# Performance work log

Hardware: AMD Instinct MI355X
Metric: run time of the kernel (lower is better)

## Reference

```python
import jax, jax.numpy as jnp
import numpy as np

QMIN_A, QMAX_A = -128, 127  # int8 activation range
GROUPSIZE = 32


def per_token_quant_dequant(x):
    """Dynamic per-token asymmetric int8 fake-quant (torchao per_token_dynamic_quant)."""
    min_val = jnp.minimum(jnp.min(x, axis=-1, keepdims=True), 0.0)
    max_val = jnp.maximum(jnp.max(x, axis=-1, keepdims=True), 0.0)
    scale = (max_val - min_val) / float(QMAX_A - QMIN_A)
    scale = jnp.maximum(scale, jnp.finfo(x.dtype).eps)
    zp = jnp.clip(QMIN_A - jnp.round(min_val / scale), QMIN_A, QMAX_A)
    q = jnp.clip(jnp.round(x / scale) + zp, QMIN_A, QMAX_A)
    return (q - zp) * scale


def dequant_int4_grouped(w_int, w_scales, w_zeros):
    """w_int: [O, I] int4 values in [-8, 7]; scales/zeros: [O, I//GROUPSIZE]."""
    O, I = w_int.shape
    G = I // GROUPSIZE
    wg = w_int.reshape(O, G, GROUPSIZE).astype(w_scales.dtype)
    w_dq = (wg - w_zeros[:, :, None]) * w_scales[:, :, None]
    return w_dq.reshape(O, I)


def setup_inputs() -> dict:
    key = jax.random.key(0)
    k1, k2, k3 = jax.random.split(key, 3)
    B, S, D_IN, D_OUT = 4, 2048, 2048, 2048
    G = D_IN // GROUPSIZE
    x = jax.random.normal(k1, (B, S, D_IN), dtype=jnp.float32)
    w_int = jax.random.randint(k2, (D_OUT, D_IN), -8, 8, dtype=jnp.int32)
    w_scales = jax.random.uniform(k3, (D_OUT, G), dtype=jnp.float32) * 0.01 + 1e-3
    w_zeros = jnp.zeros((D_OUT, G), dtype=jnp.float32)
    return {"x": x, "w_int": w_int, "w_scales": w_scales, "w_zeros": w_zeros}


def reference(x, w_int, w_scales, w_zeros):
    x_dq = per_token_quant_dequant(x)                  # [B, S, I]
    w_dq = dequant_int4_grouped(w_int, w_scales, w_zeros)  # [O, I]
    return jnp.einsum("bsi,oi->bso", x_dq, w_dq)       # [B, S, O]
```

## Files before the change

### kernel.cpp

```cpp
#include <hip/hip_runtime.h>

#define M_DIM 8192
#define N_DIM 2048
#define K_DIM 2048

#define BM 256
#define BN 128
#define BK 64

#define AS1 __attribute__((address_space(1)))
#define AS3 __attribute__((address_space(3)))

typedef float f32x4 __attribute__((ext_vector_type(4)));
typedef short s16x8 __attribute__((ext_vector_type(8)));

__device__ __forceinline__ unsigned short f2bf(float f) {
  unsigned int u = __float_as_uint(f);
  u += 0x7FFFu + ((u >> 16) & 1u);
  return (unsigned short)(u >> 16);
}

__global__ __launch_bounds__(256) void quant_x_kernel(
    const float* __restrict__ x, unsigned short* __restrict__ A) {
  const int t   = blockIdx.x;
  const int tid = threadIdx.x;
  const float4* r4 = (const float4*)(x + (size_t)t * K_DIM);
  float4 v0 = r4[tid];
  float4 v1 = r4[tid + 256];

  float mn = fminf(fminf(fminf(v0.x, v0.y), fminf(v0.z, v0.w)),
                   fminf(fminf(v1.x, v1.y), fminf(v1.z, v1.w)));
  float mx = fmaxf(fmaxf(fmaxf(v0.x, v0.y), fmaxf(v0.z, v0.w)),
                   fmaxf(fmaxf(v1.x, v1.y), fmaxf(v1.z, v1.w)));
#pragma unroll
  for (int off = 32; off > 0; off >>= 1) {
    mn = fminf(mn, __shfl_xor(mn, off));
    mx = fmaxf(mx, __shfl_xor(mx, off));
  }
  __shared__ float smn[4], smx[4];
  if ((tid & 63) == 0) { smn[tid >> 6] = mn; smx[tid >> 6] = mx; }
  __syncthreads();
  mn = fminf(fminf(smn[0], smn[1]), fminf(smn[2], smn[3]));
  mx = fmaxf(fmaxf(smx[0], smx[1]), fmaxf(smx[2], smx[3]));
  mn = fminf(mn, 0.0f);
  mx = fmaxf(mx, 0.0f);

  float scale = (mx - mn) / 255.0f;
  scale = fmaxf(scale, 1.1920928955078125e-07f);
  const float inv = 1.0f / scale;
  float zp = -128.0f - rintf(mn * inv);
  zp = fminf(fmaxf(zp, -128.0f), 127.0f);

  ushort4* Ao = (ushort4*)(A + (size_t)t * K_DIM);
  {
    float q; ushort4 r;
    q = rintf(v0.x * inv) + zp; q = fminf(fmaxf(q, -128.f), 127.f); r.x = f2bf((q - zp) * scale);
    q = rintf(v0.y * inv) + zp; q = fminf(fmaxf(q, -128.f), 127.f); r.y = f2bf((q - zp) * scale);
    q = rintf(v0.z * inv) + zp; q = fminf(fmaxf(q, -128.f), 127.f); r.z = f2bf((q - zp) * scale);
    q = rintf(v0.w * inv) + zp; q = fminf(fmaxf(q, -128.f), 127.f); r.w = f2bf((q - zp) * scale);
    Ao[tid] = r;
  }
  {
    float q; ushort4 r;
    q = rintf(v1.x * inv) + zp; q = fminf(fmaxf(q, -128.f), 127.f); r.x = f2bf((q - zp) * scale);
    q = rintf(v1.y * inv) + zp; q = fminf(fmaxf(q, -128.f), 127.f); r.y = f2bf((q - zp) * scale);
    q = rintf(v1.z * inv) + zp; q = fminf(fmaxf(q, -128.f), 127.f); r.z = f2bf((q - zp) * scale);
    q = rintf(v1.w * inv) + zp; q = fminf(fmaxf(q, -128.f), 127.f); r.w = f2bf((q - zp) * scale);
    Ao[tid + 256] = r;
  }
}

__global__ __launch_bounds__(256) void prep_w_kernel(
    const int* __restrict__ w, const float* __restrict__ ws,
    const float* __restrict__ wz, unsigned short* __restrict__ W) {
  const int idx = blockIdx.x * 256 + threadIdx.x;
  const int o  = idx >> 8;
  const int ii = (idx & 255) * 8;
  const int g  = ii >> 5;
  const float s = ws[o * 64 + g];
  const float z = wz[o * 64 + g];
  const int4* wp = (const int4*)(w + (size_t)o * K_DIM + ii);
  int4 a = wp[0], b = wp[1];
  ushort4 r0, r1;
  r0.x = f2bf(((float)a.x - z) * s);
  r0.y = f2bf(((float)a.y - z) * s);
  r0.z = f2bf(((float)a.z - z) * s);
  r0.w = f2bf(((float)a.w - z) * s);
  r1.x = f2bf(((float)b.x - z) * s);
  r1.y = f2bf(((float)b.y - z) * s);
  r1.z = f2bf(((float)b.z - z) * s);
  r1.w = f2bf(((float)b.w - z) * s);
  ushort4* Wo = (ushort4*)(W + (size_t)o * K_DIM + ii);
  Wo[0] = r0;
  Wo[1] = r1;
}

__global__ __launch_bounds__(256, 2) void gemm_kernel(
    const unsigned short* __restrict__ A,
    const unsigned short* __restrict__ B,
    float* __restrict__ C) {
  __shared__ unsigned short As[BM * BK];
  __shared__ unsigned short Bs[BN * BK];

  const int tid  = threadIdx.x;
  const int bm   = blockIdx.y * BM;
  const int bn   = blockIdx.x * BN;
  const int lane = tid & 63;
  const int wv   = tid >> 6;
  const int waveM = (wv >> 1) * 128;
  const int waveN = (wv & 1) * 64;
  const int quad = lane >> 4;
  const int l16  = lane & 15;

  const int trow = tid >> 3;
  const int phys = (tid & 7) ^ (trow & 7);
  const unsigned short* ag = A + (size_t)(bm + trow) * K_DIM + phys * 8;
  const unsigned short* bg = B + (size_t)(bn + trow) * K_DIM + phys * 8;
  unsigned short* al = &As[tid * 8];
  unsigned short* bl = &Bs[tid * 8];

  int aoff[8], boff[4];
#pragma unroll
  for (int mi = 0; mi < 8; ++mi)
    aoff[mi] = (waveM + mi * 16 + l16) * BK + ((quad ^ (l16 & 7)) * 8);
#pragma unroll
  for (int ni = 0; ni < 4; ++ni)
    boff[ni] = (waveN + ni * 16 + l16) * BK + ((quad ^ (l16 & 7)) * 8);

  f32x4 acc[8][4] = {};

  for (int k0 = 0; k0 < K_DIM; k0 += BK) {
#pragma unroll
    for (int j = 0; j < 8; ++j)
      __builtin_amdgcn_global_load_lds((const AS1 void*)(ag + (size_t)j * 32 * K_DIM + k0),
                                       (AS3 void*)(al + j * 2048), 16, 0, 0);
#pragma unroll
    for (int j = 0; j < 4; ++j)
      __builtin_amdgcn_global_load_lds((const AS1 void*)(bg + (size_t)j * 32 * K_DIM + k0),
                                       (AS3 void*)(bl + j * 2048), 16, 0, 0);
    __syncthreads();

#pragma unroll
    for (int kk = 0; kk < 2; ++kk) {
      s16x8 af[8], bf[4];
#pragma unroll
      for (int mi = 0; mi < 8; ++mi)
        af[mi] = *(const s16x8*)&As[aoff[mi] ^ (kk * 32)];
#pragma unroll
      for (int ni = 0; ni < 4; ++ni)
        bf[ni] = *(const s16x8*)&Bs[boff[ni] ^ (kk * 32)];
#pragma unroll
      for (int mi = 0; mi < 8; ++mi)
#pragma unroll
        for (int ni = 0; ni < 4; ++ni)
          acc[mi][ni] = __builtin_amdgcn_mfma_f32_16x16x32_bf16(
              af[mi], bf[ni], acc[mi][ni], 0, 0, 0);
    }
    __syncthreads();
  }

#pragma unroll
  for (int mi = 0; mi < 8; ++mi) {
#pragma unroll
    for (int ni = 0; ni < 4; ++ni) {
      const int o = bn + waveN + ni * 16 + l16;
#pragma unroll
      for (int r = 0; r < 4; ++r) {
        const int t = bm + waveM + mi * 16 + quad * 4 + r;
        C[(size_t)t * N_DIM + o] = acc[mi][ni][r];
      }
    }
  }
}

extern "C" void kernel_launch(void* const* d_in, const int* in_sizes, int n_in,
                              void* d_out, int out_size, void* d_ws, size_t ws_size,
                              hipStream_t stream) {
  const float* x        = (const float*)d_in[0];
  const int*   w_int    = (const int*)d_in[1];
  const float* w_scales = (const float*)d_in[2];
  const float* w_zeros  = (const float*)d_in[3];
  float* out = (float*)d_out;

  unsigned short* Aq = (unsigned short*)d_ws;
  unsigned short* Wq = Aq + (size_t)M_DIM * K_DIM;

  quant_x_kernel<<<M_DIM, 256, 0, stream>>>(x, Aq);
  prep_w_kernel<<<(N_DIM * (K_DIM / 8)) / 256, 256, 0, stream>>>(w_int, w_scales, w_zeros, Wq);
  dim3 grid(N_DIM / BN, M_DIM / BM);
  gemm_kernel<<<grid, 256, 0, stream>>>(Aq, Wq, out);
}
```

Measured before the change: 195.1 us.

## Double-buffer A tile, register-stage B tile, and swizzle block order

The GEMM main loop now prefetches the next K-slice while computing the current one. A is double-buffered in LDS via direct global-to-LDS loads, and B is loaded into registers and written to LDS after compute behind an extra barrier. Block indices are remapped so neighbouring workgroups share A/B tiles in cache. LDS use grows to about 80KB and register pressure rises, which may hurt the 2-blocks-per-CU occupancy target.

```diff
diff --git a/kernel.cpp b/kernel.cpp
--- a/kernel.cpp
+++ b/kernel.cpp
@@ -99,12 +99,15 @@
     const unsigned short* __restrict__ A,
     const unsigned short* __restrict__ B,
     float* __restrict__ C) {
-  __shared__ unsigned short As[BM * BK];
+  __shared__ unsigned short As[2 * BM * BK];
   __shared__ unsigned short Bs[BN * BK];
 
   const int tid  = threadIdx.x;
-  const int bm   = blockIdx.y * BM;
-  const int bn   = blockIdx.x * BN;
+  const int id  = blockIdx.y * 16 + blockIdx.x;
+  const int nid = (id & 7) * 64 + (id >> 3);
+  const int bm  = (nid >> 4) * BM;
+  const int bn  = (nid & 15) * BN;
+
   const int lane = tid & 63;
   const int wv   = tid >> 6;
   const int waveM = (wv >> 1) * 128;
@@ -115,9 +118,14 @@
   const int trow = tid >> 3;
   const int phys = (tid & 7) ^ (trow & 7);
   const unsigned short* ag = A + (size_t)(bm + trow) * K_DIM + phys * 8;
-  const unsigned short* bg = B + (size_t)(bn + trow) * K_DIM + phys * 8;
-  unsigned short* al = &As[tid * 8];
-  unsigned short* bl = &Bs[tid * 8];
+
+  const unsigned short* bgp = B + (size_t)(bn + trow) * K_DIM + (tid & 7) * 8;
+  int bwoff[4];
+#pragma unroll
+  for (int j = 0; j < 4; ++j) {
+    const int row = trow + j * 32;
+    bwoff[j] = row * BK + (((tid & 7) ^ (row & 7)) * 8);
+  }
 
   int aoff[8], boff[4];
 #pragma unroll
@@ -128,24 +136,40 @@
     boff[ni] = (waveN + ni * 16 + l16) * BK + ((quad ^ (l16 & 7)) * 8);
 
   f32x4 acc[8][4] = {};
+  s16x8 breg[4];
+
+#pragma unroll
+  for (int j = 0; j < 8; ++j)
+    __builtin_amdgcn_global_load_lds((const AS1 void*)(ag + (size_t)j * 32 * K_DIM),
+                                     (AS3 void*)(&As[tid * 8 + j * 2048]), 16, 0, 0);
+#pragma unroll
+  for (int j = 0; j < 4; ++j)
+    breg[j] = *(const s16x8*)(bgp + (size_t)j * 32 * K_DIM);
+#pragma unroll
+  for (int j = 0; j < 4; ++j)
+    *(s16x8*)&Bs[bwoff[j]] = breg[j];
+  __syncthreads();
 
   for (int k0 = 0; k0 < K_DIM; k0 += BK) {
-#pragma unroll
-    for (int j = 0; j < 8; ++j)
-      __builtin_amdgcn_global_load_lds((const AS1 void*)(ag + (size_t)j * 32 * K_DIM + k0),
-                                       (AS3 void*)(al + j * 2048), 16, 0, 0);
-#pragma unroll
-    for (int j = 0; j < 4; ++j)
-      __builtin_amdgcn_global_load_lds((const AS1 void*)(bg + (size_t)j * 32 * K_DIM + k0),
-                                       (AS3 void*)(bl + j * 2048), 16, 0, 0);
-    __syncthreads();
+    const int p  = (k0 >> 6) & 1;
+    const int kn = k0 + BK;
+    if (kn < K_DIM) {
+#pragma unroll
+      for (int j = 0; j < 8; ++j)
+        __builtin_amdgcn_global_load_lds(
+            (const AS1 void*)(ag + (size_t)j * 32 * K_DIM + kn),
+            (AS3 void*)(&As[((p ^ 1) << 14) + tid * 8 + j * 2048]), 16, 0, 0);
+#pragma unroll
+      for (int j = 0; j < 4; ++j)
+        breg[j] = *(const s16x8*)(bgp + (size_t)j * 32 * K_DIM + kn);
+    }
 
 #pragma unroll
     for (int kk = 0; kk < 2; ++kk) {
       s16x8 af[8], bf[4];
 #pragma unroll
       for (int mi = 0; mi < 8; ++mi)
-        af[mi] = *(const s16x8*)&As[aoff[mi] ^ (kk * 32)];
+        af[mi] = *(const s16x8*)&As[(p << 14) + (aoff[mi] ^ (kk * 32))];
 #pragma unroll
       for (int ni = 0; ni < 4; ++ni)
         bf[ni] = *(const s16x8*)&Bs[boff[ni] ^ (kk * 32)];
@@ -155,6 +179,12 @@
         for (int ni = 0; ni < 4; ++ni)
           acc[mi][ni] = __builtin_amdgcn_mfma_f32_16x16x32_bf16(
               af[mi], bf[ni], acc[mi][ni], 0, 0, 0);
+    }
+    __syncthreads();
+    if (kn < K_DIM) {
+#pragma unroll
+      for (int j = 0; j < 4; ++j)
+        *(s16x8*)&Bs[bwoff[j]] = breg[j];
     }
     __syncthreads();
   }
```

Measured after the change: 194.2 us. Within noise of the previous version (-0.5%).
